# Performance work log

Measured on AMD Instinct MI355X. Metric: run time of the kernel, lower is better.

The kernel has to match this reference:

```python
import jax, jax.numpy as jnp
import numpy as np

Q = 3  # q_order: SelfONN concatenates powers x^1..x^Q on channel dim

def selfonn_conv(x, w, b, pad):
    # x: (B, C, H, W); w: (O, C*Q, kh, kw); b: (O,)
    xp = jnp.concatenate([x ** (i + 1) for i in range(Q)], axis=1)
    y = jax.lax.conv_general_dilated(
        xp, w, window_strides=(1, 1), padding=[(pad, pad), (pad, pad)],
        dimension_numbers=("NCHW", "OIHW", "NCHW"))
    return y + b[None, :, None, None]

def setup_inputs() -> dict:
    key = jax.random.key(0)
    ks = jax.random.split(key, 9)
    B, C, H, W = 4, 64, 64, 64
    P = 64  # pab_channels
    s1 = 1.0 / np.sqrt(C * Q)          # 1x1 convs
    s3 = 1.0 / np.sqrt(C * Q * 9)      # 3x3 convs
    return {
        "x": jax.random.normal(ks[0], (B, C, H, W), jnp.float32),
        "top_w": jax.random.normal(ks[1], (P, C * Q, 1, 1), jnp.float32) * s1,
        "top_b": jnp.zeros((P,), jnp.float32),
        "center_w": jax.random.normal(ks[2], (P, C * Q, 1, 1), jnp.float32) * s1,
        "center_b": jnp.zeros((P,), jnp.float32),
        "bottom_w": jax.random.normal(ks[3], (C, C * Q, 3, 3), jnp.float32) * s3,
        "bottom_b": jnp.zeros((C,), jnp.float32),
        "out_w": jax.random.normal(ks[4], (C, C * Q, 3, 3), jnp.float32) * s3,
        "out_b": jnp.zeros((C,), jnp.float32),
    }

def reference(x, top_w, top_b, center_w, center_b, bottom_w, bottom_b, out_w, out_b):
    B, C, H, W = x.shape
    HW = H * W
    x_top = selfonn_conv(x, top_w, top_b, 0).reshape(B, -1, HW)            # (B, P, HW)
    x_center = selfonn_conv(x, center_w, center_b, 0).reshape(B, -1, HW)  # (B, P, HW)
    x_bottom = selfonn_conv(x, bottom_w, bottom_b, 1).reshape(B, C, HW)   # (B, C, HW)
    x_center = jnp.swapaxes(x_center, 1, 2)  # (B, HW, P)
    x_bottom = jnp.swapaxes(x_bottom, 1, 2)  # (B, HW, C)
    sp = jnp.einsum("bnp,bpm->bnm", x_center, x_top)  # (B, HW, HW)
    # GLOBAL softmax over the entire HW*HW map per sample (dim=1 on flattened view)
    sp = jax.nn.softmax(sp.reshape(B, -1), axis=1).reshape(B, HW, HW)
    sp = jnp.einsum("bnm,bmc->bnc", sp, x_bottom)  # (B, HW, C)
    # faithful to torch: raw reshape (B, HW, C) -> (B, C, H, W), no transpose
    sp = sp.reshape(B, C, H, W)
    return selfonn_conv(x + sp, out_w, out_b, 1)
```

## Files before the change

### kernel.cpp

```cpp
#include <hip/hip_runtime.h>
#include <hip/hip_bf16.h>

namespace {
constexpr int IMG    = 262144;
constexpr int PADIMG = 4356;
constexpr float LOG2E = 1.44269504088896340736f;
constexpr int WBFO  = 0;
constexpr int XPADO = 122880;
constexpr int TOPO  = 1795584;
constexpr int CENO  = 2319872;
constexpr int BOTO  = 2844160;
constexpr int PVO   = 3368448;
constexpr int MSO4  = 5465600;
constexpr int MSO8  = 7562752;
constexpr size_t NEED8 = (size_t)(MSO8 + 8192) * 4;
}

using half8v  = __attribute__((ext_vector_type(8))) _Float16;
using half4v  = __attribute__((ext_vector_type(4))) _Float16;
using short8v = __attribute__((ext_vector_type(8))) short;
using short4v = __attribute__((ext_vector_type(4))) short;
using uint4v  = __attribute__((ext_vector_type(4))) unsigned;
typedef __attribute__((ext_vector_type(4))) float f32x4;

__device__ __forceinline__ short f2bf(float f) {
    __hip_bfloat16 h = __float2bfloat16(f);
    return *reinterpret_cast<short*>(&h);
}
__device__ __forceinline__ float bf2f(short s) {
    unsigned u = ((unsigned)(unsigned short)s) << 16;
    return __uint_as_float(u);
}
__device__ __forceinline__ unsigned pkrtz(float a, float b) {
    return __builtin_bit_cast(unsigned, __builtin_amdgcn_cvt_pkrtz(a, b));
}

__global__ __launch_bounds__(256) void k_prep(const float* __restrict__ bw, const float* __restrict__ ow,
                                              const float* __restrict__ tw, const float* __restrict__ cw,
                                              _Float16* __restrict__ wbf,
                                              const float* __restrict__ x, _Float16* __restrict__ xpad) {
    __shared__ float xs[64 * 65];
    int bx = blockIdx.x, t = threadIdx.x;
    if (bx < 960) {
        int idx = bx * 256 + t;
        if (idx < 221184) {
            int tsel = idx / 110592;
            int r    = idx - tsel * 110592;
            int tap  = r / 12288;
            int rr   = r - tap * 12288;
            int ck   = rr / 2048;
            int r2   = rr - ck * 2048;
            int o    = r2 >> 5;
            int ki   = r2 & 31;
            int k    = ck * 32 + ki;
            int p    = k >> 6, ci = k & 63;
            const float* src = tsel ? ow : bw;
            wbf[idx] = (_Float16)src[o * 1728 + (p * 64 + ci) * 9 + tap];
        } else {
            int j = idx - 221184;
            int tsel = j / 12288;
            int rr   = j - tsel * 12288;
            int ck   = rr / 2048;
            int r2   = rr - ck * 2048;
            int o    = r2 >> 5;
            int ki   = r2 & 31;
            int k    = ck * 32 + ki;
            wbf[idx] = (_Float16)(tsel ? cw[o * 192 + k] * LOG2E : tw[o * 192 + k]);
        }
        return;
    }
    int bx2 = bx - 960;
    int b = bx2 >> 6, h = bx2 & 63;
    {
        _Float16* base = xpad + (size_t)b * 6 * PADIMG * 32;
        int px[6];
        px[0] = (h + 1) * 66;
        px[1] = (h + 1) * 66 + 65;
        px[2] = h;
        px[3] = 65 * 66 + h;
        int npx = 4;
        if (h < 2) { px[4] = 64 + h; px[5] = 65 * 66 + 64 + h; npx = 6; }
        int pi = t / 24, ck = t % 24;
        if (pi < npx) {
            int cp = ck >> 2, q = ck & 3;
            half8v z = {0, 0, 0, 0, 0, 0, 0, 0};
            *(half8v*)&base[((size_t)cp * PADIMG + px[pi]) * 32 + q * 8] = z;
        }
    }
    #pragma unroll
    for (int it = 0; it < 16; ++it) {
        int idx = it * 256 + t;
        int ci = idx >> 6, wc = idx & 63;
        xs[ci * 65 + wc] = x[b * IMG + ci * 4096 + h * 64 + wc];
    }
    __syncthreads();
    _Float16* dst = xpad + ((size_t)b * 6 * PADIMG + (h + 1) * 66 + 1) * 32;
    #pragma unroll
    for (int it = 0; it < 6; ++it) {
        int u = it * 256 + t;
        int ck = u >> 8, within = u & 255;
        int px = within >> 2, q = within & 3;
        int k0 = ck * 32 + q * 8;
        int p = k0 >> 6, c0 = k0 & 63;
        half8v o;
        #pragma unroll
        for (int j = 0; j < 8; ++j) {
            float v = xs[(c0 + j) * 65 + px];
            float pw = (p == 0) ? v : ((p == 1) ? v * v : v * v * v);
            o[j] = (_Float16)pw;
        }
        *(half8v*)&dst[((size_t)ck * PADIMG + px) * 32 + q * 8] = o;
    }
}

__device__ __forceinline__ void conv3d32(int bx, int t,
                                         const _Float16* __restrict__ src,
                                         const _Float16* __restrict__ wt,
                                         const float* __restrict__ bias,
                                         _Float16* __restrict__ dh_, float* __restrict__ df) {
    int lane = t & 63, w = t >> 6;
    int l16 = lane & 15, quad = lane >> 4;
    int oh = bx >> 8, mt = bx & 255;
    int b = mt >> 6, h = mt & 63;
    const _Float16* abase = src + ((size_t)b * 6 * PADIMG + (h + 1) * 66 + 1 + w * 16 + l16) * 32 + quad * 8;
    const _Float16* bbase = wt + (size_t)(oh * 32 + l16) * 32 + quad * 8;
    f32x4 acc[2];
    acc[0] = (f32x4){0.f, 0.f, 0.f, 0.f};
    acc[1] = (f32x4){0.f, 0.f, 0.f, 0.f};
    for (int tap = 0; tap < 9; ++tap) {
        int dh = tap / 3 - 1, dw = tap % 3 - 1;
        const _Float16* arow = abase + (dh * 66 + dw) * 32;
        const _Float16* brow = bbase + (size_t)tap * 6 * 2048;
        #pragma unroll
        for (int c6 = 0; c6 < 6; ++c6) {
            half8v afr  = *(const half8v*)&arow[(size_t)c6 * PADIMG * 32];
            half8v bfr0 = *(const half8v*)&brow[(size_t)c6 * 2048];
            half8v bfr1 = *(const half8v*)&brow[(size_t)c6 * 2048 + 512];
            acc[0] = __builtin_amdgcn_mfma_f32_16x16x32_f16(afr, bfr0, acc[0], 0, 0, 0);
            acc[1] = __builtin_amdgcn_mfma_f32_16x16x32_f16(afr, bfr1, acc[1], 0, 0, 0);
        }
    }
    #pragma unroll
    for (int nf = 0; nf < 2; ++nf) {
        int c = oh * 32 + nf * 16 + l16;
        float bv = bias[c];
        size_t oi = (size_t)b * 262144 + (size_t)c * 4096 + h * 64 + w * 16 + quad * 4;
        if (dh_) {
            half4v o;
            #pragma unroll
            for (int r = 0; r < 4; ++r) o[r] = (_Float16)(acc[nf][r] + bv);
            *(half4v*)&dh_[oi] = o;
        } else {
            float4 o = make_float4(acc[nf][0] + bv, acc[nf][1] + bv, acc[nf][2] + bv, acc[nf][3] + bv);
            *(float4*)&df[oi] = o;
        }
    }
}

__global__ __launch_bounds__(256) void k_convs(const _Float16* __restrict__ xpad,
                                               const _Float16* __restrict__ wbf,
                                               const float* __restrict__ tb, const float* __restrict__ cb,
                                               const float* __restrict__ bbias,
                                               _Float16* __restrict__ topd, _Float16* __restrict__ cend,
                                               _Float16* __restrict__ botb) {
    int bx = blockIdx.x, t = threadIdx.x;
    if (bx < 512) {
        conv3d32(bx, t, xpad, wbf , bbias, botb, nullptr);
        return;
    }
    int bx2 = bx - 512;
    int lane = t & 63, w = t >> 6;
    int l16 = lane & 15, quad = lane >> 4;
    int ot = bx2 >> 8, mt = bx2 & 255;
    int b = mt >> 6, h = mt & 63;
    const _Float16* wt   = wbf + (ot ? 233472 : 221184);
    const float*    bias = ot ? cb : tb;
    _Float16*       dst  = (ot ? cend : topd) + (size_t)b * IMG;
    const _Float16* abase = xpad + ((size_t)b * 6 * PADIMG + (h + 1) * 66 + 1 + w * 16 + l16) * 32 + quad * 8;
    const _Float16* bbase = wt + (size_t)l16 * 32 + quad * 8;
    f32x4 acc[4];
    #pragma unroll
    for (int nf = 0; nf < 4; ++nf) acc[nf] = (f32x4){0.f, 0.f, 0.f, 0.f};
    #pragma unroll
    for (int kc = 0; kc < 6; ++kc) {
        half8v afr = *(const half8v*)&abase[(size_t)kc * PADIMG * 32];
        #pragma unroll
        for (int nf = 0; nf < 4; ++nf) {
            half8v bfr = *(const half8v*)&bbase[(size_t)kc * 2048 + nf * 16 * 32];
            acc[nf] = __builtin_amdgcn_mfma_f32_16x16x32_f16(afr, bfr, acc[nf], 0, 0, 0);
        }
    }
    _Float16* dp = dst + (size_t)(h * 64 + w * 16) * 64;
    #pragma unroll
    for (int nf = 0; nf < 4; ++nf) {
        float bv = bias[nf * 16 + l16];
        if (ot) bv *= LOG2E;
        #pragma unroll
        for (int r = 0; r < 4; ++r)
            dp[(quad * 4 + r) * 64 + nf * 16 + l16] = (_Float16)(acc[nf][r] + bv);
    }
}

__global__ __launch_bounds__(256) void k_attn(float* __restrict__ ws, int mtiles, int msoOff, int zsoOff) {
    __shared__ _Float16 ltop[2][64 * 72];
    __shared__ _Float16 lbot[2][64 * 72];
    int t    = threadIdx.x;
    int lane = t & 63, w = t >> 6;
    int l16  = lane & 15, quad = lane >> 4;
    bool hi16 = (lane & 16) != 0;
    int bxr = blockIdx.x;
    int bx  = (bxr & 7) * ((int)gridDim.x >> 3) + (bxr >> 3);
    int st = bx & 31, b = (bx >> 5) & 3, s = bx >> 7;
    int n0 = st * 128;
    int mbase = s * mtiles * 64;
    const _Float16* topg = (const _Float16*)(ws + TOPO) + (size_t)b * IMG;
    const _Float16* ceng = (const _Float16*)(ws + CENO) + (size_t)b * IMG;
    const _Float16* botg = (const _Float16*)(ws + BOTO) + (size_t)b * IMG;

    half8v bcen[2][2];
    #pragma unroll
    for (int nj = 0; nj < 2; ++nj)
        #pragma unroll
        for (int kk = 0; kk < 2; ++kk)
            bcen[nj][kk] = *(const half8v*)&ceng[(size_t)(n0 + w * 32 + nj * 16 + l16) * 64 + kk * 32 + quad * 8];

    int r0 = t >> 3, r1 = r0 + 32, off = (t & 7) * 8;

    const half8v vone = {1, 1, 1, 1, 1, 1, 1, 1};

    f32x4 pv[4][2];
    #pragma unroll
    for (int cj = 0; cj < 4; ++cj)
        #pragma unroll
        for (int nj = 0; nj < 2; ++nj) pv[cj][nj] = (f32x4){0.f, 0.f, 0.f, 0.f};
    f32x4 zrow[2];
    zrow[0] = (f32x4){0.f, 0.f, 0.f, 0.f};
    zrow[1] = (f32x4){0.f, 0.f, 0.f, 0.f};
    float runm = -3.0e38f;

    half8v rt0 = *(const half8v*)&topg[(size_t)(mbase + r0) * 64 + off];
    half8v rt1 = *(const half8v*)&topg[(size_t)(mbase + r1) * 64 + off];
    half8v rb0 = *(const half8v*)&botg[(size_t)r0 * 4096 + mbase + off];
    half8v rb1 = *(const half8v*)&botg[(size_t)r1 * 4096 + mbase + off];

    for (int tt = 0; tt < mtiles; ++tt) {
        _Float16* lt = ltop[tt & 1];
        _Float16* lb = lbot[tt & 1];
        *(half8v*)&lt[r0 * 72 + off] = rt0;
        *(half8v*)&lt[r1 * 72 + off] = rt1;
        *(half8v*)&lb[r0 * 72 + off] = rb0;
        *(half8v*)&lb[r1 * 72 + off] = rb1;
        __syncthreads();
        if (tt + 1 < mtiles) {
            int m1 = mbase + (tt + 1) * 64;
            rt0 = *(const half8v*)&topg[(size_t)(m1 + r0) * 64 + off];
            rt1 = *(const half8v*)&topg[(size_t)(m1 + r1) * 64 + off];
            rb0 = *(const half8v*)&botg[(size_t)r0 * 4096 + m1 + off];
            rb1 = *(const half8v*)&botg[(size_t)r1 * 4096 + m1 + off];
        }
        f32x4 sa[4][2];
        #pragma unroll
        for (int mi = 0; mi < 4; ++mi)
            #pragma unroll
            for (int nj = 0; nj < 2; ++nj) sa[mi][nj] = (f32x4){0.f, 0.f, 0.f, 0.f};
        __builtin_amdgcn_s_setprio(1);
        #pragma unroll
        for (int kk = 0; kk < 2; ++kk)
            #pragma unroll
            for (int mi = 0; mi < 4; ++mi) {
                half8v at = *(half8v*)&lt[(mi * 16 + l16) * 72 + kk * 32 + quad * 8];
                sa[mi][0] = __builtin_amdgcn_mfma_f32_16x16x32_f16(at, bcen[0][kk], sa[mi][0], 0, 0, 0);
                sa[mi][1] = __builtin_amdgcn_mfma_f32_16x16x32_f16(at, bcen[1][kk], sa[mi][1], 0, 0, 0);
            }
        __builtin_amdgcn_s_setprio(0);
        float lm = -3.0e38f;
        #pragma unroll
        for (int mi = 0; mi < 4; ++mi)
            #pragma unroll
            for (int nj = 0; nj < 2; ++nj) {
                float a  = fmaxf(sa[mi][nj][0], sa[mi][nj][1]);
                float c2 = fmaxf(sa[mi][nj][2], sa[mi][nj][3]);
                lm = fmaxf(lm, fmaxf(a, c2));
            }
        if (!__all(lm - runm <= 8.0f)) {
            float tm = lm;
            for (int o2 = 32; o2; o2 >>= 1) tm = fmaxf(tm, __shfl_xor(tm, o2, 64));
            if (tm > runm) {
                float sc = __builtin_amdgcn_exp2f(runm - tm);
                #pragma unroll
                for (int cj = 0; cj < 4; ++cj)
                    #pragma unroll
                    for (int nj = 0; nj < 2; ++nj) pv[cj][nj] *= sc;
                zrow[0] *= sc;
                zrow[1] *= sc;
                runm = tm;
            }
        }
        #pragma unroll
        for (int kb = 0; kb < 2; ++kb) {
            unsigned pk[2][2][2];
            #pragma unroll
            for (int f = 0; f < 2; ++f) {
                int mi = 2 * kb + f;
                #pragma unroll
                for (int nj = 0; nj < 2; ++nj) {
                    float e0 = __builtin_amdgcn_exp2f(sa[mi][nj][0] - runm);
                    float e1 = __builtin_amdgcn_exp2f(sa[mi][nj][1] - runm);
                    float e2 = __builtin_amdgcn_exp2f(sa[mi][nj][2] - runm);
                    float e3 = __builtin_amdgcn_exp2f(sa[mi][nj][3] - runm);
                    pk[f][nj][0] = pkrtz(e0, e1);
                    pk[f][nj][1] = pkrtz(e2, e3);
                }
            }
            half8v pa[2];
            #pragma unroll
            for (int nj = 0; nj < 2; ++nj) {
                unsigned T[4];
                #pragma unroll
                for (int d = 0; d < 2; ++d) {
                    unsigned X = pk[0][nj][d], Y = pk[1][nj][d];
                    asm("v_permlane32_swap_b32 %0, %1" : "+v"(X), "+v"(Y));
                    unsigned A0s = __builtin_amdgcn_ds_swizzle(X, 0x401F);
                    unsigned A1s = __builtin_amdgcn_ds_swizzle(Y, 0x401F);
                    T[d]     = hi16 ? A1s : X;
                    T[d + 2] = hi16 ? Y : A0s;
                }
                uint4v tv = {T[0], T[1], T[2], T[3]};
                pa[nj] = __builtin_bit_cast(half8v, tv);
            }
            __builtin_amdgcn_s_setprio(1);
            #pragma unroll
            for (int cj = 0; cj < 4; ++cj) {
                half8v ab = *(half8v*)&lb[(cj * 16 + l16) * 72 + kb * 32 + quad * 8];
                pv[cj][0] = __builtin_amdgcn_mfma_f32_16x16x32_f16(ab, pa[0], pv[cj][0], 0, 0, 0);
                pv[cj][1] = __builtin_amdgcn_mfma_f32_16x16x32_f16(ab, pa[1], pv[cj][1], 0, 0, 0);
            }
            zrow[0] = __builtin_amdgcn_mfma_f32_16x16x32_f16(vone, pa[0], zrow[0], 0, 0, 0);
            zrow[1] = __builtin_amdgcn_mfma_f32_16x16x32_f16(vone, pa[1], zrow[1], 0, 0, 0);
            __builtin_amdgcn_s_setprio(0);
        }
    }
    float zacc = (zrow[0][0] + zrow[1][0]) * 0.25f;
    for (int o2 = 32; o2; o2 >>= 1) zacc += __shfl_xor(zacc, o2, 64);
    if (lane == 0) {
        ws[msoOff + s * 512 + b * 128 + st * 4 + w] = runm;
        ws[zsoOff + s * 512 + b * 128 + st * 4 + w] = zacc;
    }
    short* pvp = (short*)(ws + PVO) + (size_t)s * 1048576 + (size_t)b * IMG;
    #pragma unroll
    for (int cj = 0; cj < 4; ++cj)
        #pragma unroll
        for (int nj = 0; nj < 2; ++nj) {
            short4v o;
            #pragma unroll
            for (int r = 0; r < 4; ++r) o[r] = f2bf(pv[cj][nj][r]);
            *(short4v*)&pvp[(size_t)(n0 + w * 32 + nj * 16 + l16) * 64 + cj * 16 + quad * 4] = o;
        }
}

__global__ __launch_bounds__(512) void k_finalu(const float* __restrict__ x, float* __restrict__ ws,
                                                _Float16* __restrict__ upad,
                                                int ms, int msoOff, int zsoOff) {
    __shared__ float us[64 * 65];
    __shared__ float rm[8], rz[8];
    int t = threadIdx.x, bx = blockIdx.x;
    int b = bx >> 6, h = bx & 63;
    int g = t & 127;
    float m = -3.0e38f;
    for (int s = 0; s < ms; ++s)
        m = fmaxf(m, ws[msoOff + s * 512 + b * 128 + g]);
    for (int o2 = 32; o2; o2 >>= 1) m = fmaxf(m, __shfl_xor(m, o2, 64));
    if ((t & 63) == 0) rm[t >> 6] = m;
    __syncthreads();
    float M = rm[0];
    #pragma unroll
    for (int j = 1; j < 8; ++j) M = fmaxf(M, rm[j]);
    float z = 0.f;
    if (t < 128) {
        for (int s = 0; s < ms; ++s)
            z += ws[zsoOff + s * 512 + b * 128 + g] *
                 __builtin_amdgcn_exp2f(ws[msoOff + s * 512 + b * 128 + g] - M);
    }
    for (int o2 = 32; o2; o2 >>= 1) z += __shfl_xor(z, o2, 64);
    if ((t & 63) == 0) rz[t >> 6] = z;
    __syncthreads();
    float Z = 0.f;
    #pragma unroll
    for (int j = 0; j < 8; ++j) Z += rz[j];
    float rZ = 1.0f / Z;

    const short* pvb = (const short*)(ws + PVO) + (size_t)b * IMG;
    int hg = h >> 5;
    {
        int idx = t * 8;
        int ci = idx >> 6, wc = idx & 63;
        int rem = ci * 4096 + h * 64 + wc;
        int grp = ci * 2 + hg;
        float acc[8] = {};
        for (int s = 0; s < ms; ++s) {
            float scl = __builtin_amdgcn_exp2f(ws[msoOff + s * 512 + b * 128 + grp] - M);
            short8v pvv = *(const short8v*)&pvb[(size_t)s * 1048576 + rem];
            #pragma unroll
            for (int i = 0; i < 8; ++i) acc[i] += bf2f(pvv[i]) * scl;
        }
        float4 x0 = *(const float4*)&x[(size_t)b * IMG + rem];
        float4 x1 = *(const float4*)&x[(size_t)b * IMG + rem + 4];
        float xv[8] = {x0.x, x0.y, x0.z, x0.w, x1.x, x1.y, x1.z, x1.w};
        #pragma unroll
        for (int i = 0; i < 8; ++i)
            us[ci * 65 + wc + i] = xv[i] + acc[i] * rZ;
    }
    __syncthreads();
    _Float16* dst = upad + ((size_t)b * 6 * PADIMG + (h + 1) * 66 + 1) * 32;
    #pragma unroll
    for (int it = 0; it < 3; ++it) {
        int u = it * 512 + t;
        int ck = u >> 8, within = u & 255;
        int px = within >> 2, q = within & 3;
        int k0 = ck * 32 + q * 8;
        int p = k0 >> 6, c0 = k0 & 63;
        half8v o;
        #pragma unroll
        for (int j = 0; j < 8; ++j) {
            float v = us[(c0 + j) * 65 + px];
            float pw = (p == 0) ? v : ((p == 1) ? v * v : v * v * v);
            o[j] = (_Float16)pw;
        }
        *(half8v*)&dst[((size_t)ck * PADIMG + px) * 32 + q * 8] = o;
    }
}

__global__ __launch_bounds__(256) void k_conv3o(const _Float16* __restrict__ upad,
                                                const _Float16* __restrict__ wout,
                                                const float* __restrict__ ob,
                                                float* __restrict__ out) {
    conv3d32(blockIdx.x, threadIdx.x, upad, wout, ob, nullptr, out);
}

extern "C" void kernel_launch(void* const* d_in, const int* in_sizes, int n_in,
                              void* d_out, int out_size, void* d_ws, size_t ws_size,
                              hipStream_t stream) {
    (void)in_sizes; (void)n_in; (void)out_size;
    const float* x  = (const float*)d_in[0];
    const float* tw = (const float*)d_in[1];
    const float* tb = (const float*)d_in[2];
    const float* cw = (const float*)d_in[3];
    const float* cb = (const float*)d_in[4];
    const float* bw = (const float*)d_in[5];
    const float* bb = (const float*)d_in[6];
    const float* ow = (const float*)d_in[7];
    const float* ob = (const float*)d_in[8];
    float* ws  = (float*)d_ws;
    float* out = (float*)d_out;

    _Float16* wbf  = (_Float16*)(ws + WBFO);
    _Float16* wout = wbf + 110592;
    _Float16* xpad = (_Float16*)(ws + XPADO);
    _Float16* topb = (_Float16*)(ws + TOPO);
    _Float16* cenb = (_Float16*)(ws + CENO);
    _Float16* botb = (_Float16*)(ws + BOTO);

    int ms     = (ws_size >= NEED8) ? 8 : 4;
    int mtiles = 64 / ms;
    int msoOff = (ms == 8) ? MSO8 : MSO4;
    int zsoOff = msoOff + ms * 512;

    hipLaunchKernelGGL(k_prep, dim3(1216), dim3(256), 0, stream, bw, ow, tw, cw, wbf, x, xpad);
    hipLaunchKernelGGL(k_convs, dim3(1024), dim3(256), 0, stream, xpad, wbf, tb, cb, bb, topb, cenb, botb);
    hipLaunchKernelGGL(k_attn, dim3(128 * ms), dim3(256), 0, stream, ws, mtiles, msoOff, zsoOff);
    hipLaunchKernelGGL(k_finalu, dim3(256), dim3(512), 0, stream, x, ws, xpad, ms, msoOff, zsoOff);
    hipLaunchKernelGGL(k_conv3o, dim3(512), dim3(256), 0, stream, xpad, wout, ob, out);
}
```

Before: 166.4 us.

## Template attention tile count, stagger block starts, use permlane16 swap

Makes the attention kernel's tile count a template parameter so the main loop is fully unrolled. Adds s_sleep delays that grow with a block-index slot, so groups of blocks start their load and compute phases out of phase. Replaces the two ds_swizzle calls and lane selects in the P-fragment transpose with a single v_permlane16_swap instruction. The staggering adds idle cycles at block start, and full unrolling may raise register pressure.

```diff
diff --git a/kernel.cpp b/kernel.cpp
--- a/kernel.cpp
+++ b/kernel.cpp
@@ -201,18 +201,24 @@
     }
 }
 
-__global__ __launch_bounds__(256) void k_attn(float* __restrict__ ws, int mtiles, int msoOff, int zsoOff) {
+template<int MT>
+__global__ __launch_bounds__(256) void k_attn(float* __restrict__ ws, int msoOff, int zsoOff) {
     __shared__ _Float16 ltop[2][64 * 72];
     __shared__ _Float16 lbot[2][64 * 72];
     int t    = threadIdx.x;
     int lane = t & 63, w = t >> 6;
     int l16  = lane & 15, quad = lane >> 4;
-    bool hi16 = (lane & 16) != 0;
     int bxr = blockIdx.x;
+    {
+        int slot = (bxr >> 8) & 3;
+        if (slot == 1)      __builtin_amdgcn_s_sleep(24);
+        else if (slot == 2) __builtin_amdgcn_s_sleep(48);
+        else if (slot == 3) __builtin_amdgcn_s_sleep(72);
+    }
     int bx  = (bxr & 7) * ((int)gridDim.x >> 3) + (bxr >> 3);
     int st = bx & 31, b = (bx >> 5) & 3, s = bx >> 7;
     int n0 = st * 128;
-    int mbase = s * mtiles * 64;
+    int mbase = s * MT * 64;
     const _Float16* topg = (const _Float16*)(ws + TOPO) + (size_t)b * IMG;
     const _Float16* ceng = (const _Float16*)(ws + CENO) + (size_t)b * IMG;
     const _Float16* botg = (const _Float16*)(ws + BOTO) + (size_t)b * IMG;
@@ -243,7 +249,8 @@
     half8v rb0 = *(const half8v*)&botg[(size_t)r0 * 4096 + mbase + off];
     half8v rb1 = *(const half8v*)&botg[(size_t)r1 * 4096 + mbase + off];
 
-    for (int tt = 0; tt < mtiles; ++tt) {
+    #pragma unroll
+    for (int tt = 0; tt < MT; ++tt) {
         _Float16* lt = ltop[tt & 1];
         _Float16* lb = lbot[tt & 1];
         *(half8v*)&lt[r0 * 72 + off] = rt0;
@@ -251,7 +258,7 @@
         *(half8v*)&lb[r0 * 72 + off] = rb0;
         *(half8v*)&lb[r1 * 72 + off] = rb1;
         __syncthreads();
-        if (tt + 1 < mtiles) {
+        if (tt + 1 < MT) {
             int m1 = mbase + (tt + 1) * 64;
             rt0 = *(const half8v*)&topg[(size_t)(m1 + r0) * 64 + off];
             rt1 = *(const half8v*)&topg[(size_t)(m1 + r1) * 64 + off];
@@ -320,10 +327,9 @@
                 for (int d = 0; d < 2; ++d) {
                     unsigned X = pk[0][nj][d], Y = pk[1][nj][d];
                     asm("v_permlane32_swap_b32 %0, %1" : "+v"(X), "+v"(Y));
-                    unsigned A0s = __builtin_amdgcn_ds_swizzle(X, 0x401F);
-                    unsigned A1s = __builtin_amdgcn_ds_swizzle(Y, 0x401F);
-                    T[d]     = hi16 ? A1s : X;
-                    T[d + 2] = hi16 ? Y : A0s;
+                    asm("v_permlane16_swap_b32 %0, %1" : "+v"(X), "+v"(Y));
+                    T[d]     = X;
+                    T[d + 2] = Y;
                 }
                 uint4v tv = {T[0], T[1], T[2], T[3]};
                 pa[nj] = __builtin_bit_cast(half8v, tv);
@@ -461,13 +467,15 @@
     _Float16* botb = (_Float16*)(ws + BOTO);
 
     int ms     = (ws_size >= NEED8) ? 8 : 4;
-    int mtiles = 64 / ms;
     int msoOff = (ms == 8) ? MSO8 : MSO4;
     int zsoOff = msoOff + ms * 512;
 
     hipLaunchKernelGGL(k_prep, dim3(1216), dim3(256), 0, stream, bw, ow, tw, cw, wbf, x, xpad);
     hipLaunchKernelGGL(k_convs, dim3(1024), dim3(256), 0, stream, xpad, wbf, tb, cb, bb, topb, cenb, botb);
-    hipLaunchKernelGGL(k_attn, dim3(128 * ms), dim3(256), 0, stream, ws, mtiles, msoOff, zsoOff);
+    if (ms == 8)
+        hipLaunchKernelGGL(k_attn<8>,  dim3(1024), dim3(256), 0, stream, ws, msoOff, zsoOff);
+    else
+        hipLaunchKernelGGL(k_attn<16>, dim3(512),  dim3(256), 0, stream, ws, msoOff, zsoOff);
     hipLaunchKernelGGL(k_finalu, dim3(256), dim3(512), 0, stream, x, ws, xpad, ms, msoOff, zsoOff);
     hipLaunchKernelGGL(k_conv3o, dim3(512), dim3(256), 0, stream, xpad, wout, ob, out);
 }
```

Measured after the change: 165.6 us. No clear change (-0.5%).
